# Kernel tuning notes

Measured on AMD Instinct MI355X. Metric: run time of the kernel, lower is better.

The kernel has to match this reference:

```python
import jax, jax.numpy as jnp
import numpy as np

N = 500000
D = 128
R = D // 4  # reduction = 4
G = 2048    # number of graphs


def setup_inputs() -> dict:
    key = jax.random.key(0)
    ks = jax.random.split(key, 8)
    x = jax.random.normal(ks[0], (N, D), dtype=jnp.float32)
    batch = jnp.sort(jax.random.randint(ks[1], (N,), 0, G))
    # SE-gate MLP params (nn.Linear stores weight as [out,in]; we store transposed for x @ W)
    fc_w1 = jax.random.normal(ks[2], (D, R), dtype=jnp.float32) * (1.0 / np.sqrt(D))
    fc_b1 = jnp.zeros((R,), dtype=jnp.float32)
    fc_w2 = jax.random.normal(ks[3], (R, D), dtype=jnp.float32) * (1.0 / np.sqrt(R))
    fc_b2 = jnp.zeros((D,), dtype=jnp.float32)
    # xavier-uniform weight_matrix [D, D]
    lim = np.sqrt(6.0 / (D + D))
    W = jax.random.uniform(ks[4], (D, D), dtype=jnp.float32, minval=-lim, maxval=lim)
    return {"x": x, "batch": batch, "size": G,
            "fc_w1": fc_w1, "fc_b1": fc_b1, "fc_w2": fc_w2, "fc_b2": fc_b2, "W": W}


def reference(x, batch, size, fc_w1, fc_b1, fc_w2, fc_b2, W):
    # gated SE-block: attention = tanh(MLP(x)); x = attention*x + x
    attention = jnp.tanh(jnp.maximum(x @ fc_w1 + fc_b1, 0.0) @ fc_w2 + fc_b2)
    x2 = attention * x + x  # [N, D]
    # global_mean_pool: segment mean over graphs
    seg_sum = jax.ops.segment_sum(x2, batch, num_segments=size)           # [G, D]
    counts = jax.ops.segment_sum(jnp.ones((x2.shape[0],), x2.dtype), batch, num_segments=size)
    mean = seg_sum / jnp.maximum(counts, 1.0)[:, None]                     # [G, D]
    transformed_global = jnp.tanh(mean @ W)                                # [G, D]
    # gather-broadcast per-graph global back to nodes, per-node attention coef
    coefs = jax.nn.sigmoid(jnp.sum(x2 * transformed_global[batch], axis=1))  # [N]
    weighted = coefs[:, None] * x2                                          # [N, D]
    return jax.ops.segment_sum(weighted, batch, num_segments=size)          # [G, D]
```

## Files before the change

### kernel.cpp

```cpp
#include <hip/hip_runtime.h>
#include <hip/hip_bf16.h>

#define DDIM 128
#define RDIM 32
#define PBLK 256
#define BLK  256
#define HSTR 32

typedef __attribute__((ext_vector_type(8))) short bf16x8;
typedef __attribute__((ext_vector_type(4))) float f32x4;

__device__ __forceinline__ float tanh_fast(float v) {
  float e = __expf(2.f * v);
  return 1.f - 2.f * __builtin_amdgcn_rcpf(e + 1.f);
}
__device__ __forceinline__ float sigmoid_fast(float v) {
  return __builtin_amdgcn_rcpf(1.f + __expf(-v));
}
__device__ __forceinline__ unsigned short f2bf(float f) {
  unsigned u = __float_as_uint(f);
  u += 0x7fffu + ((u >> 16) & 1u);
  return (unsigned short)(u >> 16);
}
__device__ __forceinline__ float bf2f(unsigned short s) {
  return __uint_as_float(((unsigned)s) << 16);
}
__device__ __forceinline__ unsigned pkbf(float lo, float hi) {
  __hip_bfloat162 t2 = __float22bfloat162_rn(make_float2(lo, hi));
  return *reinterpret_cast<unsigned*>(&t2);
}
__device__ __forceinline__ int lower_bound(const int* __restrict__ b, int n, int v) {
  int lo = 0, hi = n;
  while (lo < hi) { int m = (lo + hi) >> 1; if (b[m] < v) lo = m + 1; else hi = m; }
  return lo;
}

__global__ void k0_prep(const float* __restrict__ w1, const float* __restrict__ w2,
                        unsigned short* __restrict__ w1tf, unsigned short* __restrict__ w2tf)
{
  const int i  = blockIdx.x * blockDim.x + threadIdx.x;
  const int l  = i & 63;
  const int lr = l & 15, q = l >> 4;
  if (i < 512) {
    const int frag = i >> 6;
    const int mt2 = frag >> 2, kk = frag & 3;
    bf16x8 v;
    #pragma unroll
    for (int j = 0; j < 8; ++j)
      v[j] = (short)f2bf(w1[(size_t)(kk * 32 + q * 8 + j) * RDIM + mt2 * 16 + lr]);
    *(bf16x8*)&w1tf[(size_t)i * 8] = v;
  } else {
    const int mt = (i - 512) >> 6;
    bf16x8 v;
    #pragma unroll
    for (int j = 0; j < 8; ++j)
      v[j] = (short)f2bf(w2[(size_t)(q * 8 + j) * DDIM + mt * 16 + lr]);
    *(bf16x8*)&w2tf[(size_t)(i - 512) * 8] = v;
  }
}

__global__ void kb_bounds(const int* __restrict__ batch, int* __restrict__ bounds,
                          int N, int G)
{
  const int g = blockIdx.x * blockDim.x + threadIdx.x;
  if (g <= G) bounds[g] = lower_bound(batch, N, g);
}

__global__ __launch_bounds__(BLK, 3) void k_fused(
    const float* __restrict__ x,
    const unsigned short* __restrict__ w1tf, const float* __restrict__ b1,
    const unsigned short* __restrict__ w2tf, const float* __restrict__ b2,
    const float* __restrict__ W, const int* __restrict__ bounds,
    float* __restrict__ out, int N)
{
  __shared__ unsigned short w1t[512 * 8];
  __shared__ unsigned short w2t[512 * 8];
  __shared__ float slots[4][2048];
  __shared__ unsigned short hs4[4][16 * HSTR];
  __shared__ float b2s[DDIM];
  __shared__ float tgs[DDIM];

  const int t  = threadIdx.x;
  const int l  = t & 63;
  const int w  = t >> 6;
  const int lr = l & 15;
  const int q  = l >> 4;
  const int g  = blockIdx.x;
  const int lo = bounds[g], hi = bounds[g + 1];
  const int cnt = hi - lo;
  unsigned short* hs = hs4[w];
  float* slot = slots[w];
  float (*part)[132] = (float (*)[132])slots[0];
  float* meanv = slots[1];

  if (cnt <= 0) { if (t < DDIM) out[(size_t)g * DDIM + t] = 0.f; return; }

  for (int i = t; i < 512; i += BLK) {
    ((bf16x8*)w1t)[i] = ((const bf16x8*)w1tf)[i];
    ((bf16x8*)w2t)[i] = ((const bf16x8*)w2tf)[i];
  }
  if (t < DDIM) b2s[t] = b2[t];
  const float4 b1q0 = *(const float4*)(b1 + q * 4);
  const float4 b1q1 = *(const float4*)(b1 + 16 + q * 4);
  __syncthreads();

  const int sr  = l >> 5;
  const int sc  = l & 31;
  const int swz = lr & 7;
  const int ntile = (cnt + 15) >> 4;

  auto fill = [&](int tb) {
    #pragma unroll
    for (int j = 0; j < 8; ++j) {
      const int r   = j * 2 + sr;
      const int row = lo + min(tb + r, cnt - 1);
      const int lc  = sc ^ (r & 7);
      __builtin_amdgcn_global_load_lds(x + (size_t)row * DDIM + lc * 4,
                                       slot + j * 256, 16, 0, 0);
    }
  };

  auto loadregs = [&](bf16x8 (&xf)[4], uint2 (&xg)[8]) {
    #pragma unroll
    for (int kk = 0; kk < 4; ++kk) {
      const int c0 = kk * 8 + q * 2;
      float4 a = *(const float4*)&slot[lr * 128 + ((c0    ) ^ swz) * 4];
      float4 b = *(const float4*)&slot[lr * 128 + ((c0 + 1) ^ swz) * 4];
      uint4 u;
      u.x = pkbf(a.x, a.y); u.y = pkbf(a.z, a.w);
      u.z = pkbf(b.x, b.y); u.w = pkbf(b.z, b.w);
      xf[kk] = *(bf16x8*)&u;
    }
    #pragma unroll
    for (int mt = 0; mt < 8; ++mt) {
      float4 v = *(const float4*)&slot[lr * 128 + ((mt * 4 + q) ^ swz) * 4];
      xg[mt].x = pkbf(v.x, v.y); xg[mt].y = pkbf(v.z, v.w);
    }
  };

  auto compute = [&](const bf16x8 (&xf)[4], const uint2 (&xg)[8],
                     f32x4 (&cacc)[8]) {
    f32x4 hacc[2];
    hacc[0][0] = b1q0.x; hacc[0][1] = b1q0.y; hacc[0][2] = b1q0.z; hacc[0][3] = b1q0.w;
    hacc[1][0] = b1q1.x; hacc[1][1] = b1q1.y; hacc[1][2] = b1q1.z; hacc[1][3] = b1q1.w;
    #pragma unroll
    for (int kk = 0; kk < 4; ++kk) {
      bf16x8 wa = *(const bf16x8*)&w1t[(size_t)((0 * 4 + kk) * 64 + l) * 8];
      bf16x8 wb = *(const bf16x8*)&w1t[(size_t)((1 * 4 + kk) * 64 + l) * 8];
      hacc[0] = __builtin_amdgcn_mfma_f32_16x16x32_bf16(wa, xf[kk], hacc[0], 0, 0, 0);
      hacc[1] = __builtin_amdgcn_mfma_f32_16x16x32_bf16(wb, xf[kk], hacc[1], 0, 0, 0);
    }
    #pragma unroll
    for (int mt2 = 0; mt2 < 2; ++mt2) {
      float h0 = fmaxf(hacc[mt2][0], 0.f), h1 = fmaxf(hacc[mt2][1], 0.f);
      float h2 = fmaxf(hacc[mt2][2], 0.f), h3 = fmaxf(hacc[mt2][3], 0.f);
      uint2 p; p.x = pkbf(h0, h1); p.y = pkbf(h2, h3);
      *(uint2*)&hs[lr * HSTR + mt2 * 16 + q * 4] = p;
    }
    bf16x8 ah = *(const bf16x8*)&hs[lr * HSTR + q * 8];
    #pragma unroll
    for (int mt = 0; mt < 8; ++mt) {
      float4 bv = *(const float4*)&b2s[mt * 16 + q * 4];
      cacc[mt][0] = bv.x; cacc[mt][1] = bv.y; cacc[mt][2] = bv.z; cacc[mt][3] = bv.w;
    }
    #pragma unroll
    for (int mt = 0; mt < 8; ++mt) {
      bf16x8 wf = *(const bf16x8*)&w2t[(size_t)(mt * 64 + l) * 8];
      cacc[mt] = __builtin_amdgcn_mfma_f32_16x16x32_bf16(wf, ah, cacc[mt], 0, 0, 0);
    }
    #pragma unroll
    for (int mt = 0; mt < 8; ++mt) {
      float x0 = bf2f((unsigned short)(xg[mt].x & 0xffffu));
      float x1 = bf2f((unsigned short)(xg[mt].x >> 16));
      float x2 = bf2f((unsigned short)(xg[mt].y & 0xffffu));
      float x3 = bf2f((unsigned short)(xg[mt].y >> 16));
      cacc[mt][0] = x0 * (1.f + tanh_fast(cacc[mt][0]));
      cacc[mt][1] = x1 * (1.f + tanh_fast(cacc[mt][1]));
      cacc[mt][2] = x2 * (1.f + tanh_fast(cacc[mt][2]));
      cacc[mt][3] = x3 * (1.f + tanh_fast(cacc[mt][3]));
    }
  };

  float macc[8][4];
  #pragma unroll
  for (int mt = 0; mt < 8; ++mt)
    #pragma unroll
    for (int c = 0; c < 4; ++c) macc[mt][c] = 0.f;

  {
    int ti = w;
    if (ti < ntile) fill(ti * 16);
    for (; ti < ntile; ti += 4) {
      asm volatile("s_waitcnt vmcnt(0)" ::: "memory");
      bf16x8 xf[4]; uint2 xg[8];
      loadregs(xf, xg);
      asm volatile("s_waitcnt lgkmcnt(0)" ::: "memory");
      if (ti + 4 < ntile) fill((ti + 4) * 16);
      f32x4 cacc[8];
      compute(xf, xg, cacc);
      if (ti * 16 + lr < cnt) {
        #pragma unroll
        for (int mt = 0; mt < 8; ++mt)
          #pragma unroll
          for (int c = 0; c < 4; ++c) macc[mt][c] += cacc[mt][c];
      }
    }
  }
  __syncthreads();

  #pragma unroll
  for (int mt = 0; mt < 8; ++mt)
    #pragma unroll
    for (int c = 0; c < 4; ++c) {
      float v = macc[mt][c];
      v += __shfl_xor(v, 1, 64);
      v += __shfl_xor(v, 2, 64);
      v += __shfl_xor(v, 4, 64);
      v += __shfl_xor(v, 8, 64);
      macc[mt][c] = v;
    }
  if (lr == 0) {
    #pragma unroll
    for (int mt = 0; mt < 8; ++mt)
      *(float4*)&part[w][mt * 16 + q * 4] =
          make_float4(macc[mt][0], macc[mt][1], macc[mt][2], macc[mt][3]);
  }
  __syncthreads();
  if (t < DDIM) {
    float m = part[0][t] + part[1][t] + part[2][t] + part[3][t];
    meanv[t] = m / (float)cnt;
  }
  __syncthreads();

  {
    const int c = t & 127, s = t >> 7;
    float a = 0.f;
    #pragma unroll 8
    for (int k = 0; k < 64; ++k)
      a = fmaf(meanv[s * 64 + k], W[(size_t)(s * 64 + k) * DDIM + c], a);
    part[s][c] = a;
  }
  __syncthreads();
  if (t < DDIM) tgs[t] = tanh_fast(part[0][t] + part[1][t]);
  __syncthreads();

  float oacc[8][4];
  #pragma unroll
  for (int mt = 0; mt < 8; ++mt)
    #pragma unroll
    for (int c = 0; c < 4; ++c) oacc[mt][c] = 0.f;

  {
    int ti = w;
    if (ti < ntile) fill(ti * 16);
    for (; ti < ntile; ti += 4) {
      asm volatile("s_waitcnt vmcnt(0)" ::: "memory");
      bf16x8 xf[4]; uint2 xg[8];
      loadregs(xf, xg);
      asm volatile("s_waitcnt lgkmcnt(0)" ::: "memory");
      if (ti + 4 < ntile) fill((ti + 4) * 16);
      f32x4 cacc[8];
      compute(xf, xg, cacc);
      float p = 0.f;
      #pragma unroll
      for (int mt = 0; mt < 8; ++mt) {
        float4 tg4 = *(const float4*)&tgs[mt * 16 + q * 4];
        p = fmaf(cacc[mt][0], tg4.x, p); p = fmaf(cacc[mt][1], tg4.y, p);
        p = fmaf(cacc[mt][2], tg4.z, p); p = fmaf(cacc[mt][3], tg4.w, p);
      }
      p += __shfl_xor(p, 16, 64);
      p += __shfl_xor(p, 32, 64);
      const float coef = sigmoid_fast(p);
      if (ti * 16 + lr < cnt) {
        #pragma unroll
        for (int mt = 0; mt < 8; ++mt)
          #pragma unroll
          for (int c = 0; c < 4; ++c)
            oacc[mt][c] = fmaf(coef, cacc[mt][c], oacc[mt][c]);
      }
    }
  }
  __syncthreads();

  #pragma unroll
  for (int mt = 0; mt < 8; ++mt)
    #pragma unroll
    for (int c = 0; c < 4; ++c) {
      float v = oacc[mt][c];
      v += __shfl_xor(v, 1, 64);
      v += __shfl_xor(v, 2, 64);
      v += __shfl_xor(v, 4, 64);
      v += __shfl_xor(v, 8, 64);
      oacc[mt][c] = v;
    }
  if (lr == 0) {
    #pragma unroll
    for (int mt = 0; mt < 8; ++mt)
      *(float4*)&part[w][mt * 16 + q * 4] =
          make_float4(oacc[mt][0], oacc[mt][1], oacc[mt][2], oacc[mt][3]);
  }
  __syncthreads();
  if (t < DDIM)
    out[(size_t)g * DDIM + t] = part[0][t] + part[1][t] + part[2][t] + part[3][t];
}

extern "C" void kernel_launch(void* const* d_in, const int* in_sizes, int n_in,
                              void* d_out, int out_size, void* d_ws, size_t ws_size,
                              hipStream_t stream) {
  const float* x     = (const float*)d_in[0];
  const int*   batch = (const int*)d_in[1];
  const float* w1 = (const float*)d_in[3];
  const float* b1 = (const float*)d_in[4];
  const float* w2 = (const float*)d_in[5];
  const float* b2 = (const float*)d_in[6];
  const float* W  = (const float*)d_in[7];
  float* out = (float*)d_out;

  const int N = in_sizes[0] / DDIM;
  const int G = out_size / DDIM;

  unsigned short* w1tf = (unsigned short*)d_ws;
  unsigned short* w2tf = w1tf + 4096;
  int* bounds = (int*)(w2tf + 4096);
  (void)ws_size; (void)n_in;

  hipLaunchKernelGGL(k0_prep, dim3(4), dim3(PBLK), 0, stream, w1, w2, w1tf, w2tf);
  hipLaunchKernelGGL(kb_bounds, dim3((G + 1 + PBLK - 1) / PBLK), dim3(PBLK), 0, stream,
                     batch, bounds, N, G);
  hipLaunchKernelGGL(k_fused, dim3(G), dim3(BLK), 0, stream,
                     x, w1tf, b1, w2tf, b2, W, bounds, out, N);
}
```

Baseline: 150.9 us.

## Double-buffer per-wave LDS tiles and keep MLP weights in registers

Each wave now gets a two-slot LDS ring, so the tile two steps ahead is fetched while the next tile is read into registers and the current one is computed, deepening the load pipeline. The MLP weight fragments move from shared memory into registers held for the whole kernel, removing LDS reads from the MFMA loop. The hidden scratch stride is padded to 40 to avoid bank conflicts, and launch bounds drop to 2 blocks per CU to make room for the extra registers and LDS. Lower occupancy and higher register pressure are the risks.

```diff
diff --git a/kernel.cpp b/kernel.cpp
--- a/kernel.cpp
+++ b/kernel.cpp
@@ -5,7 +5,7 @@
 #define RDIM 32
 #define PBLK 256
 #define BLK  256
-#define HSTR 32
+#define HSTR 40
 
 typedef __attribute__((ext_vector_type(8))) short bf16x8;
 typedef __attribute__((ext_vector_type(4))) float f32x4;
@@ -66,19 +66,19 @@
   if (g <= G) bounds[g] = lower_bound(batch, N, g);
 }
 
-__global__ __launch_bounds__(BLK, 3) void k_fused(
+__global__ __launch_bounds__(BLK, 2) void k_fused(
     const float* __restrict__ x,
     const unsigned short* __restrict__ w1tf, const float* __restrict__ b1,
     const unsigned short* __restrict__ w2tf, const float* __restrict__ b2,
     const float* __restrict__ W, const int* __restrict__ bounds,
     float* __restrict__ out, int N)
 {
-  __shared__ unsigned short w1t[512 * 8];
-  __shared__ unsigned short w2t[512 * 8];
-  __shared__ float slots[4][2048];
+  __shared__ float ring[4][2][2048];
   __shared__ unsigned short hs4[4][16 * HSTR];
+  __shared__ float part[4][132];
+  __shared__ float meanv[DDIM];
+  __shared__ float tgs[DDIM];
   __shared__ float b2s[DDIM];
-  __shared__ float tgs[DDIM];
 
   const int t  = threadIdx.x;
   const int l  = t & 63;
@@ -89,19 +89,22 @@
   const int lo = bounds[g], hi = bounds[g + 1];
   const int cnt = hi - lo;
   unsigned short* hs = hs4[w];
-  float* slot = slots[w];
-  float (*part)[132] = (float (*)[132])slots[0];
-  float* meanv = slots[1];
 
   if (cnt <= 0) { if (t < DDIM) out[(size_t)g * DDIM + t] = 0.f; return; }
 
-  for (int i = t; i < 512; i += BLK) {
-    ((bf16x8*)w1t)[i] = ((const bf16x8*)w1tf)[i];
-    ((bf16x8*)w2t)[i] = ((const bf16x8*)w2tf)[i];
-  }
-  if (t < DDIM) b2s[t] = b2[t];
+  bf16x8 w1r[2][4], w2r[8];
+  #pragma unroll
+  for (int mt2 = 0; mt2 < 2; ++mt2)
+    #pragma unroll
+    for (int kk = 0; kk < 4; ++kk)
+      w1r[mt2][kk] = *(const bf16x8*)&w1tf[(size_t)((mt2 * 4 + kk) * 64 + l) * 8];
+  #pragma unroll
+  for (int mt = 0; mt < 8; ++mt)
+    w2r[mt] = *(const bf16x8*)&w2tf[(size_t)(mt * 64 + l) * 8];
+
   const float4 b1q0 = *(const float4*)(b1 + q * 4);
   const float4 b1q1 = *(const float4*)(b1 + 16 + q * 4);
+  if (t < DDIM) b2s[t] = b2[t];
   __syncthreads();
 
   const int sr  = l >> 5;
@@ -109,23 +112,25 @@
   const int swz = lr & 7;
   const int ntile = (cnt + 15) >> 4;
 
-  auto fill = [&](int tb) {
+  auto fill = [&](int s, int tb) {
+    float* lds = ring[w][s];
     #pragma unroll
     for (int j = 0; j < 8; ++j) {
       const int r   = j * 2 + sr;
       const int row = lo + min(tb + r, cnt - 1);
       const int lc  = sc ^ (r & 7);
       __builtin_amdgcn_global_load_lds(x + (size_t)row * DDIM + lc * 4,
-                                       slot + j * 256, 16, 0, 0);
+                                       lds + j * 256, 16, 0, 0);
     }
   };
 
-  auto loadregs = [&](bf16x8 (&xf)[4], uint2 (&xg)[8]) {
+  auto loadregs = [&](int s, bf16x8 (&xf)[4], uint2 (&xg)[8]) {
+    float* lds = ring[w][s];
     #pragma unroll
     for (int kk = 0; kk < 4; ++kk) {
       const int c0 = kk * 8 + q * 2;
-      float4 a = *(const float4*)&slot[lr * 128 + ((c0    ) ^ swz) * 4];
-      float4 b = *(const float4*)&slot[lr * 128 + ((c0 + 1) ^ swz) * 4];
+      float4 a = *(const float4*)&lds[lr * 128 + ((c0    ) ^ swz) * 4];
+      float4 b = *(const float4*)&lds[lr * 128 + ((c0 + 1) ^ swz) * 4];
       uint4 u;
       u.x = pkbf(a.x, a.y); u.y = pkbf(a.z, a.w);
       u.z = pkbf(b.x, b.y); u.w = pkbf(b.z, b.w);
@@ -133,7 +138,7 @@
     }
     #pragma unroll
     for (int mt = 0; mt < 8; ++mt) {
-      float4 v = *(const float4*)&slot[lr * 128 + ((mt * 4 + q) ^ swz) * 4];
+      float4 v = *(const float4*)&lds[lr * 128 + ((mt * 4 + q) ^ swz) * 4];
       xg[mt].x = pkbf(v.x, v.y); xg[mt].y = pkbf(v.z, v.w);
     }
   };
@@ -145,10 +150,8 @@
     hacc[1][0] = b1q1.x; hacc[1][1] = b1q1.y; hacc[1][2] = b1q1.z; hacc[1][3] = b1q1.w;
     #pragma unroll
     for (int kk = 0; kk < 4; ++kk) {
-      bf16x8 wa = *(const bf16x8*)&w1t[(size_t)((0 * 4 + kk) * 64 + l) * 8];
-      bf16x8 wb = *(const bf16x8*)&w1t[(size_t)((1 * 4 + kk) * 64 + l) * 8];
-      hacc[0] = __builtin_amdgcn_mfma_f32_16x16x32_bf16(wa, xf[kk], hacc[0], 0, 0, 0);
-      hacc[1] = __builtin_amdgcn_mfma_f32_16x16x32_bf16(wb, xf[kk], hacc[1], 0, 0, 0);
+      hacc[0] = __builtin_amdgcn_mfma_f32_16x16x32_bf16(w1r[0][kk], xf[kk], hacc[0], 0, 0, 0);
+      hacc[1] = __builtin_amdgcn_mfma_f32_16x16x32_bf16(w1r[1][kk], xf[kk], hacc[1], 0, 0, 0);
     }
     #pragma unroll
     for (int mt2 = 0; mt2 < 2; ++mt2) {
@@ -164,10 +167,8 @@
       cacc[mt][0] = bv.x; cacc[mt][1] = bv.y; cacc[mt][2] = bv.z; cacc[mt][3] = bv.w;
     }
     #pragma unroll
-    for (int mt = 0; mt < 8; ++mt) {
-      bf16x8 wf = *(const bf16x8*)&w2t[(size_t)(mt * 64 + l) * 8];
-      cacc[mt] = __builtin_amdgcn_mfma_f32_16x16x32_bf16(wf, ah, cacc[mt], 0, 0, 0);
-    }
+    for (int mt = 0; mt < 8; ++mt)
+      cacc[mt] = __builtin_amdgcn_mfma_f32_16x16x32_bf16(w2r[mt], ah, cacc[mt], 0, 0, 0);
     #pragma unroll
     for (int mt = 0; mt < 8; ++mt) {
       float x0 = bf2f((unsigned short)(xg[mt].x & 0xffffu));
@@ -181,6 +182,20 @@
     }
   };
 
+  auto step = [&](int ti, int p,
+                  const bf16x8 (&xfC)[4], const uint2 (&xgC)[8],
+                  bf16x8 (&xfN)[4], uint2 (&xgN)[8], f32x4 (&cacc)[8]) {
+    asm volatile("s_waitcnt lgkmcnt(0)" ::: "memory");
+    if (ti + 8 < ntile) {
+      fill(p, (ti + 8) * 16);
+      asm volatile("s_waitcnt vmcnt(8)" ::: "memory");
+    } else if (ti + 4 < ntile) {
+      asm volatile("s_waitcnt vmcnt(0)" ::: "memory");
+    }
+    if (ti + 4 < ntile) loadregs(p ^ 1, xfN, xgN);
+    compute(xfC, xgC, cacc);
+  };
+
   float macc[8][4];
   #pragma unroll
   for (int mt = 0; mt < 8; ++mt)
@@ -188,22 +203,26 @@
     for (int c = 0; c < 4; ++c) macc[mt][c] = 0.f;
 
   {
+    bf16x8 xfA[4], xfB[4]; uint2 xgA[8], xgB[8];
     int ti = w;
-    if (ti < ntile) fill(ti * 16);
-    for (; ti < ntile; ti += 4) {
+    if (ti < ntile) {
+      fill(0, ti * 16);
       asm volatile("s_waitcnt vmcnt(0)" ::: "memory");
-      bf16x8 xf[4]; uint2 xg[8];
-      loadregs(xf, xg);
-      asm volatile("s_waitcnt lgkmcnt(0)" ::: "memory");
-      if (ti + 4 < ntile) fill((ti + 4) * 16);
+      loadregs(0, xfA, xgA);
+      if (ti + 4 < ntile) fill(1, (ti + 4) * 16);
+    }
+    int p = 0;
+    while (ti < ntile) {
       f32x4 cacc[8];
-      compute(xf, xg, cacc);
+      if (p == 0) step(ti, 0, xfA, xgA, xfB, xgB, cacc);
+      else        step(ti, 1, xfB, xgB, xfA, xgA, cacc);
       if (ti * 16 + lr < cnt) {
         #pragma unroll
         for (int mt = 0; mt < 8; ++mt)
           #pragma unroll
           for (int c = 0; c < 4; ++c) macc[mt][c] += cacc[mt][c];
       }
+      ti += 4; p ^= 1;
     }
   }
   __syncthreads();
@@ -251,26 +270,29 @@
     for (int c = 0; c < 4; ++c) oacc[mt][c] = 0.f;
 
   {
+    bf16x8 xfA[4], xfB[4]; uint2 xgA[8], xgB[8];
     int ti = w;
-    if (ti < ntile) fill(ti * 16);
-    for (; ti < ntile; ti += 4) {
+    if (ti < ntile) {
+      fill(0, ti * 16);
       asm volatile("s_waitcnt vmcnt(0)" ::: "memory");
-      bf16x8 xf[4]; uint2 xg[8];
-      loadregs(xf, xg);
-      asm volatile("s_waitcnt lgkmcnt(0)" ::: "memory");
-      if (ti + 4 < ntile) fill((ti + 4) * 16);
+      loadregs(0, xfA, xgA);
+      if (ti + 4 < ntile) fill(1, (ti + 4) * 16);
+    }
+    int p = 0;
+    while (ti < ntile) {
       f32x4 cacc[8];
-      compute(xf, xg, cacc);
-      float p = 0.f;
+      if (p == 0) step(ti, 0, xfA, xgA, xfB, xgB, cacc);
+      else        step(ti, 1, xfB, xgB, xfA, xgA, cacc);
+      float pp = 0.f;
       #pragma unroll
       for (int mt = 0; mt < 8; ++mt) {
         float4 tg4 = *(const float4*)&tgs[mt * 16 + q * 4];
-        p = fmaf(cacc[mt][0], tg4.x, p); p = fmaf(cacc[mt][1], tg4.y, p);
-        p = fmaf(cacc[mt][2], tg4.z, p); p = fmaf(cacc[mt][3], tg4.w, p);
+        pp = fmaf(cacc[mt][0], tg4.x, pp); pp = fmaf(cacc[mt][1], tg4.y, pp);
+        pp = fmaf(cacc[mt][2], tg4.z, pp); pp = fmaf(cacc[mt][3], tg4.w, pp);
       }
-      p += __shfl_xor(p, 16, 64);
-      p += __shfl_xor(p, 32, 64);
-      const float coef = sigmoid_fast(p);
+      pp += __shfl_xor(pp, 16, 64);
+      pp += __shfl_xor(pp, 32, 64);
+      const float coef = sigmoid_fast(pp);
       if (ti * 16 + lr < cnt) {
         #pragma unroll
         for (int mt = 0; mt < 8; ++mt)
@@ -278,6 +300,7 @@
           for (int c = 0; c < 4; ++c)
             oacc[mt][c] = fmaf(coef, cacc[mt][c], oacc[mt][c]);
       }
+      ti += 4; p ^= 1;
     }
   }
   __syncthreads();
```

After: 356.3 us. 2.36x slower.
